# Performance work log

Measured on AMD Instinct MI355X. Metric: run time of the kernel, lower is better.

The kernel has to match this reference:

```python
import jax, jax.numpy as jnp
import numpy as np

B, S, D, H = 4, 2048, 512, 8
NEG_INF = -1e9


def setup_inputs() -> dict:
    key = jax.random.key(0)
    ks = jax.random.split(key, 5)
    x = jax.random.normal(ks[0], (B, S, D), dtype=jnp.float32)
    mask = jnp.ones((B, S), dtype=jnp.int32)
    sc = 0.04  # ~1/sqrt(D) init scale
    Wq = jax.random.normal(ks[1], (H, D, D), dtype=jnp.float32) * sc
    Wk = jax.random.normal(ks[2], (H, D, D), dtype=jnp.float32) * sc
    Wv = jax.random.normal(ks[3], (H, D, D), dtype=jnp.float32) * sc
    Wp = jax.random.normal(ks[4], (D, H * D), dtype=jnp.float32) * sc
    return {"x": x, "mask": mask, "Wq": Wq, "Wk": Wk, "Wv": Wv, "Wp": Wp}


def reference(x, mask, Wq, Wk, Wv, Wp):
    d = x.shape[-1]
    scale = 1.0 / jnp.sqrt(jnp.asarray(d, dtype=jnp.float32))
    # torch Linear: y = x @ W.T ; per-head full-width projections
    q = jnp.einsum("bsd,hed->bhse", x, Wq)  # [B,H,S,D]
    k = jnp.einsum("bsd,hed->bhse", x, Wk)
    v = jnp.einsum("bsd,hed->bhse", x, Wv)
    logits = jnp.einsum("bhse,bhte->bhst", q, k) * scale  # [B,H,S,S]
    # pairwise mask = outer product mask[:,:,None] @ mask[:,None,:]
    pair = (mask[:, :, None] * mask[:, None, :])[:, None, :, :]  # [B,1,S,S]
    logits = jnp.where(pair > 0, logits, NEG_INF)
    attn = jax.nn.softmax(logits, axis=-1)
    out = jnp.einsum("bhst,bhte->bhse", attn, v)  # [B,H,S,D]
    # concat heads along last dim (head order preserved) then proj (no bias)
    bsz, h, s, dd = out.shape
    cat = jnp.transpose(out, (0, 2, 1, 3)).reshape(bsz, s, h * dd)
    return jnp.einsum("bsf,df->bsd", cat, Wp)
```

## Files before the change

kernel.cpp:

```cpp
#include <hip/hip_runtime.h>
#include <hip/hip_bf16.h>


using bf16x8 = __attribute__((ext_vector_type(8))) short;
using f32x4  = __attribute__((ext_vector_type(4))) float;
typedef unsigned short u16;

__device__ __forceinline__ u16 f2bf(float f) {
  union { float f; unsigned u; } c; c.f = f;
  unsigned r = c.u + 0x7fffu + ((c.u >> 16) & 1u);
  return (u16)(r >> 16);
}

__device__ __forceinline__ void gload16(const void* g, void* l) {
  __builtin_amdgcn_global_load_lds((const __attribute__((address_space(1))) unsigned int*)g,
                                   (__attribute__((address_space(3))) unsigned int*)l, 16, 0, 0);
}

__global__ void k_cvt(const float* __restrict__ s, u16* __restrict__ d, int n4) {
  int i = blockIdx.x * 256 + threadIdx.x;
  if (i >= n4) return;
  float4 v = reinterpret_cast<const float4*>(s)[i];
  ushort4 o;
  o.x = f2bf(v.x); o.y = f2bf(v.y); o.z = f2bf(v.z); o.w = f2bf(v.w);
  reinterpret_cast<ushort4*>(d)[i] = o;
}

__global__ __launch_bounds__(256) void k_gemm_qkv(
    const u16* __restrict__ xb, const u16* __restrict__ w,
    u16* __restrict__ Qc, u16* __restrict__ Kc, u16* __restrict__ VTc,
    int h0, int HC)
{
  __shared__ u16 As[128][32];
  __shared__ u16 Bs[128][32];

  const int m0 = blockIdx.x * 128;
  const int n0 = blockIdx.y * 128;
  const int zz = blockIdx.z;
  const int t  = zz / HC, hr = zz % HC;
  const int h  = h0 + hr;

  const int tid  = threadIdx.x;
  const int lane = tid & 63, wv = tid >> 6;
  const int wr = (wv >> 1) * 64, wc = (wv & 1) * 64;
  const int r16 = lane & 15, kg = lane >> 4;

  const u16* wbase = w + (size_t)(t * 8 + h) * 512 * 512;
  const int strow = tid >> 2;
  const int sc4   = (tid & 3) * 8;

  const u16* gaa = xb    + (size_t)(m0 + strow) * 512 + sc4;
  const u16* gbb = wbase + (size_t)(n0 + strow) * 512 + sc4;
  char* AsB = (char*)&As[0][0] + wv * 1024;
  char* BsB = (char*)&Bs[0][0] + wv * 1024;

  f32x4 acc[4][4];
  f32x4 zero = {0.f, 0.f, 0.f, 0.f};
#pragma unroll
  for (int i = 0; i < 4; ++i)
#pragma unroll
    for (int j = 0; j < 4; ++j) acc[i][j] = zero;

  for (int kt = 0; kt < 16; ++kt) {
    __syncthreads();
    const int ko = kt * 32;
    gload16(gaa + ko,            AsB);
    gload16(gaa + 64 * 512 + ko, AsB + 4096);
    gload16(gbb + ko,            BsB);
    gload16(gbb + 64 * 512 + ko, BsB + 4096);
    __syncthreads();
    bf16x8 af[4], bfv[4];
#pragma unroll
    for (int i = 0; i < 4; ++i) af[i]  = *(const bf16x8*)&As[wr + i * 16 + r16][kg * 8];
#pragma unroll
    for (int j = 0; j < 4; ++j) bfv[j] = *(const bf16x8*)&Bs[wc + j * 16 + r16][kg * 8];
#pragma unroll
    for (int i = 0; i < 4; ++i)
#pragma unroll
      for (int j = 0; j < 4; ++j)
        acc[i][j] = __builtin_amdgcn_mfma_f32_16x16x32_bf16(af[i], bfv[j], acc[i][j], 0, 0, 0);
  }

#pragma unroll
  for (int i = 0; i < 4; ++i) {
    const int mbase = m0 + wr + i * 16 + kg * 4;
    const int b   = mbase >> 11;
    const int sl  = mbase & 2047;
    const int bhc = b * HC + hr;
#pragma unroll
    for (int j = 0; j < 4; ++j) {
      const int col = n0 + wc + j * 16 + r16;
      if (t == 2) {
        ushort4 o;
        o.x = f2bf(acc[i][j][0]); o.y = f2bf(acc[i][j][1]);
        o.z = f2bf(acc[i][j][2]); o.w = f2bf(acc[i][j][3]);
        *(ushort4*)&VTc[((size_t)bhc * 512 + col) * 2048 + sl] = o;
      } else if (t == 1) {
#pragma unroll
        for (int q = 0; q < 4; ++q) {
          const int s   = sl + q;
          const int row = s & 63;
          const size_t idx = ((size_t)bhc << 20)
                           + (size_t)((s >> 6) * 4 + (col >> 7)) * 8192
                           + row * 128 + ((col & 127) ^ ((row & 7) << 3));
          Kc[idx] = f2bf(acc[i][j][q]);
        }
      } else {
#pragma unroll
        for (int q = 0; q < 4; ++q)
          Qc[((size_t)bhc * 2048 + sl + q) * 512 + col] = f2bf(acc[i][j][q]);
      }
    }
  }
}

__global__ __launch_bounds__(256) void k_attn(
    const u16* __restrict__ Qc, const u16* __restrict__ Kc, const u16* __restrict__ VTc,
    const int* __restrict__ mask, u16* __restrict__ catc, int HC)
{
  __shared__ u16  Qs[32 * 512];
  __shared__ u16  Ks[2 * 8192];
  __shared__ float S_lds[32][68];
  __shared__ u16  P_lds[32][72];
  __shared__ float m_run[32], l_run[32], alpha_s[32];

  const int lin = blockIdx.x + (blockIdx.y << 6);
  const int per = (gridDim.y << 6) >> 3;
  const int nl  = (lin & 7) * per + (lin >> 3);
  const int qt  = nl & 63, bhc = nl >> 6;

  const int b = bhc / HC, hr = bhc % HC;
  const int q0 = qt * 32;

  const int tid = threadIdx.x, lane = tid & 63, wv = tid >> 6;
  const int r16 = lane & 15, kg = lane >> 4;

  const u16* Qg = Qc + ((size_t)bhc * 2048 + q0) * 512;
  const u16* Kg = Kc + ((size_t)bhc << 20);
  const u16* Vg = VTc + (size_t)bhc * 512 * 2048;
  const int* mrow = mask + b * 2048;

  for (int s = tid; s < 2048; s += 256) {
    const int row = s >> 6, col = (s & 63) * 8;
    *(int4*)&Qs[row * 512 + (col ^ ((row & 7) << 3))] =
        *(const int4*)(Qg + row * 512 + col);
  }
  if (tid < 32) { m_run[tid] = -__builtin_inff(); l_run[tid] = 0.f; }

  auto kissue = [&](int gi, int cur) {
    const u16* g = Kg + (size_t)gi * 8192 + wv * 2048 + lane * 8;
    u16* l = &Ks[cur * 8192 + wv * 2048];
#pragma unroll
    for (int r = 0; r < 4; ++r)
      gload16(g + r * 512, l + r * 512);
  };

  kissue(0, 0);
  kissue(1, 1);

  asm volatile("s_waitcnt lgkmcnt(0)" ::: "memory");
  __builtin_amdgcn_s_barrier();

  const int sm_row = tid >> 3, sm_c0 = (tid & 7) * 8;
  const int rm = mrow[q0 + sm_row];
  const int krow = wv * 16 + r16;
  const int kswz = (krow & 7) << 3;

  f32x4 acc[2][8];
  f32x4 zero = {0.f, 0.f, 0.f, 0.f};
#pragma unroll
  for (int mi = 0; mi < 2; ++mi)
#pragma unroll
    for (int nf = 0; nf < 8; ++nf) acc[mi][nf] = zero;

  const float scale = 0.044194173824159216f;

  for (int it = 0; it < 32; ++it) {
    const int t0 = it * 64;
    f32x4 sacc[2] = {zero, zero};

#pragma unroll
    for (int c = 0; c < 4; ++c) {
      const int gi = it * 4 + c;
      const int cur = gi & 1;
      asm volatile("s_waitcnt vmcnt(4)" ::: "memory");
      __builtin_amdgcn_s_setprio(1);
#pragma unroll
      for (int ks = 0; ks < 4; ++ks) {
        bf16x8 kb = *(const bf16x8*)&Ks[cur * 8192 + krow * 128 + ((ks * 32 + kg * 8) ^ kswz)];
#pragma unroll
        for (int mi = 0; mi < 2; ++mi) {
          const int qrow = mi * 16 + r16;
          bf16x8 qa = *(const bf16x8*)&Qs[qrow * 512 +
              ((c * 128 + ks * 32 + kg * 8) ^ ((qrow & 7) << 3))];
          sacc[mi] = __builtin_amdgcn_mfma_f32_16x16x32_bf16(qa, kb, sacc[mi], 0, 0, 0);
        }
      }
      __builtin_amdgcn_s_setprio(0);
      if (c == 3) {
#pragma unroll
        for (int mi = 0; mi < 2; ++mi)
#pragma unroll
          for (int q = 0; q < 4; ++q)
            S_lds[mi * 16 + kg * 4 + q][wv * 16 + r16] = sacc[mi][q];
      }
      asm volatile("s_waitcnt lgkmcnt(0)" ::: "memory");
      __builtin_amdgcn_sched_barrier(0);
      if (gi + 2 < 128) kissue(gi + 2, cur);
    }
    __builtin_amdgcn_s_barrier();

    bf16x8 vfrag[2][8];
#pragma unroll
    for (int ks = 0; ks < 2; ++ks)
#pragma unroll
      for (int nf = 0; nf < 8; ++nf)
        vfrag[ks][nf] = *(const bf16x8*)(Vg +
            (size_t)(wv * 128 + nf * 16 + r16) * 2048 + t0 + ks * 32 + kg * 8);

    {
      float4 sA = *(float4*)&S_lds[sm_row][sm_c0];
      float4 sB = *(float4*)&S_lds[sm_row][sm_c0 + 4];
      const int4 cA = *(const int4*)(mrow + t0 + sm_c0);
      const int4 cB = *(const int4*)(mrow + t0 + sm_c0 + 4);
      float s0 = (rm && cA.x) ? sA.x * scale : -1e9f;
      float s1 = (rm && cA.y) ? sA.y * scale : -1e9f;
      float s2 = (rm && cA.z) ? sA.z * scale : -1e9f;
      float s3 = (rm && cA.w) ? sA.w * scale : -1e9f;
      float s4 = (rm && cB.x) ? sB.x * scale : -1e9f;
      float s5 = (rm && cB.y) ? sB.y * scale : -1e9f;
      float s6 = (rm && cB.z) ? sB.z * scale : -1e9f;
      float s7 = (rm && cB.w) ? sB.w * scale : -1e9f;
      float mt = fmaxf(fmaxf(fmaxf(s0, s1), fmaxf(s2, s3)),
                       fmaxf(fmaxf(s4, s5), fmaxf(s6, s7)));
      mt = fmaxf(mt, __shfl_xor(mt, 1));
      mt = fmaxf(mt, __shfl_xor(mt, 2));
      mt = fmaxf(mt, __shfl_xor(mt, 4));
      const float mo = m_run[sm_row];
      const float mn = fmaxf(mo, mt);
      const float al = __expf(mo - mn);
      float p0 = __expf(s0 - mn), p1 = __expf(s1 - mn);
      float p2 = __expf(s2 - mn), p3 = __expf(s3 - mn);
      float p4 = __expf(s4 - mn), p5 = __expf(s5 - mn);
      float p6 = __expf(s6 - mn), p7 = __expf(s7 - mn);
      float ps = ((p0 + p1) + (p2 + p3)) + ((p4 + p5) + (p6 + p7));
      ps += __shfl_xor(ps, 1); ps += __shfl_xor(ps, 2); ps += __shfl_xor(ps, 4);
      ushort4 w0, w1;
      w0.x = f2bf(p0); w0.y = f2bf(p1); w0.z = f2bf(p2); w0.w = f2bf(p3);
      w1.x = f2bf(p4); w1.y = f2bf(p5); w1.z = f2bf(p6); w1.w = f2bf(p7);
      *(ushort4*)&P_lds[sm_row][sm_c0]     = w0;
      *(ushort4*)&P_lds[sm_row][sm_c0 + 4] = w1;
      if ((tid & 7) == 0) {
        m_run[sm_row] = mn;
        l_run[sm_row] = l_run[sm_row] * al + ps;
        alpha_s[sm_row] = al;
      }
    }
    asm volatile("s_waitcnt lgkmcnt(0)" ::: "memory");
    __builtin_amdgcn_s_barrier();

    float alq[2][4];
#pragma unroll
    for (int mi = 0; mi < 2; ++mi)
#pragma unroll
      for (int q = 0; q < 4; ++q) alq[mi][q] = alpha_s[mi * 16 + kg * 4 + q];
#pragma unroll
    for (int mi = 0; mi < 2; ++mi)
#pragma unroll
      for (int nf = 0; nf < 8; ++nf) {
        acc[mi][nf][0] *= alq[mi][0]; acc[mi][nf][1] *= alq[mi][1];
        acc[mi][nf][2] *= alq[mi][2]; acc[mi][nf][3] *= alq[mi][3];
      }
    __builtin_amdgcn_s_setprio(1);
#pragma unroll
    for (int ks = 0; ks < 2; ++ks) {
      bf16x8 pa0 = *(const bf16x8*)&P_lds[r16][ks * 32 + kg * 8];
      bf16x8 pa1 = *(const bf16x8*)&P_lds[16 + r16][ks * 32 + kg * 8];
#pragma unroll
      for (int nf = 0; nf < 8; ++nf) {
        acc[0][nf] = __builtin_amdgcn_mfma_f32_16x16x32_bf16(pa0, vfrag[ks][nf], acc[0][nf], 0, 0, 0);
        acc[1][nf] = __builtin_amdgcn_mfma_f32_16x16x32_bf16(pa1, vfrag[ks][nf], acc[1][nf], 0, 0, 0);
      }
    }
    __builtin_amdgcn_s_setprio(0);
  }

  float rinv[2][4];
#pragma unroll
  for (int mi = 0; mi < 2; ++mi)
#pragma unroll
    for (int q = 0; q < 4; ++q) rinv[mi][q] = 1.0f / l_run[mi * 16 + kg * 4 + q];
  const int ldc = HC * 512;
#pragma unroll
  for (int mi = 0; mi < 2; ++mi)
#pragma unroll
    for (int nf = 0; nf < 8; ++nf) {
      const int col = hr * 512 + wv * 128 + nf * 16 + r16;
#pragma unroll
      for (int q = 0; q < 4; ++q) {
        const int row = b * 2048 + q0 + mi * 16 + kg * 4 + q;
        catc[(size_t)row * ldc + col] = f2bf(acc[mi][nf][q] * rinv[mi][q]);
      }
    }
}

__global__ __launch_bounds__(256) void k_gemm_out(
    const u16* __restrict__ A, const u16* __restrict__ Bw, float* __restrict__ out,
    int HC, int h0, int init)
{
  __shared__ u16 As[128][32];
  __shared__ u16 Bs[128][32];

  const int m0 = blockIdx.x * 128;
  const int n0 = blockIdx.y * 128;
  const int tid = threadIdx.x, lane = tid & 63, wv = tid >> 6;
  const int wr = (wv >> 1) * 64, wc = (wv & 1) * 64;
  const int r16 = lane & 15, kg = lane >> 4;
  const int strow = tid >> 2, sc4 = (tid & 3) * 8;
  const size_t lda = (size_t)HC * 512;
  const int nkt = HC * 16;

  const u16* gaa = A  + (size_t)(m0 + strow) * lda + sc4;
  const u16* gbb = Bw + (size_t)(n0 + strow) * 4096 + h0 * 512 + sc4;
  char* AsB = (char*)&As[0][0] + wv * 1024;
  char* BsB = (char*)&Bs[0][0] + wv * 1024;

  f32x4 acc[4][4];
  f32x4 zero = {0.f, 0.f, 0.f, 0.f};
#pragma unroll
  for (int i = 0; i < 4; ++i)
#pragma unroll
    for (int j = 0; j < 4; ++j) acc[i][j] = zero;

  for (int kt = 0; kt < nkt; ++kt) {
    __syncthreads();
    const int ko = kt * 32;
    gload16(gaa + ko,            AsB);
    gload16(gaa + 64 * lda + ko, AsB + 4096);
    gload16(gbb + ko,            BsB);
    gload16(gbb + (size_t)64 * 4096 + ko, BsB + 4096);
    __syncthreads();
    bf16x8 af[4], bfv[4];
#pragma unroll
    for (int i = 0; i < 4; ++i) af[i]  = *(const bf16x8*)&As[wr + i * 16 + r16][kg * 8];
#pragma unroll
    for (int j = 0; j < 4; ++j) bfv[j] = *(const bf16x8*)&Bs[wc + j * 16 + r16][kg * 8];
#pragma unroll
    for (int i = 0; i < 4; ++i)
#pragma unroll
      for (int j = 0; j < 4; ++j)
        acc[i][j] = __builtin_amdgcn_mfma_f32_16x16x32_bf16(af[i], bfv[j], acc[i][j], 0, 0, 0);
  }

#pragma unroll
  for (int i = 0; i < 4; ++i)
#pragma unroll
    for (int j = 0; j < 4; ++j) {
      const int col = n0 + wc + j * 16 + r16;
#pragma unroll
      for (int q = 0; q < 4; ++q) {
        const int row = m0 + wr + i * 16 + kg * 4 + q;
        if (init) out[(size_t)row * 512 + col] = acc[i][j][q];
        else      out[(size_t)row * 512 + col] += acc[i][j][q];
      }
    }
}

extern "C" void kernel_launch(void* const* d_in, const int* in_sizes, int n_in,
                              void* d_out, int out_size, void* d_ws, size_t ws_size,
                              hipStream_t stream)
{
  (void)in_sizes; (void)n_in; (void)out_size;
  const float* x  = (const float*)d_in[0];
  const int* mask = (const int*)d_in[1];
  const float* Wq = (const float*)d_in[2];
  const float* Wk = (const float*)d_in[3];
  const float* Wv = (const float*)d_in[4];
  const float* Wp = (const float*)d_in[5];

  const size_t MiB = 1024 * 1024;
  int HC = 1;
  if (ws_size >= 24 * MiB + 32 * 8 * MiB)      HC = 8;
  else if (ws_size >= 24 * MiB + 32 * 4 * MiB) HC = 4;
  else if (ws_size >= 24 * MiB + 32 * 2 * MiB) HC = 2;

  char* ws = (char*)d_ws;
  size_t off = 0;
  u16* xb   = (u16*)(ws + off); off += 8 * MiB;
  u16* wqkv = (u16*)(ws + off); off += 12 * MiB;
  u16* wpb  = (u16*)(ws + off); off += 4 * MiB;
  const size_t qsz = (size_t)4 * HC * 2048 * 512 * 2;
  u16* Qc  = (u16*)(ws + off); off += qsz;
  u16* Kc  = (u16*)(ws + off); off += qsz;
  u16* VTc = (u16*)(ws + off); off += qsz;
  u16* catc = (u16*)(ws + off);

  k_cvt<<<4096, 256, 0, stream>>>(x,  xb, 1048576);
  k_cvt<<<2048, 256, 0, stream>>>(Wq, wqkv,           524288);
  k_cvt<<<2048, 256, 0, stream>>>(Wk, wqkv + 2097152, 524288);
  k_cvt<<<2048, 256, 0, stream>>>(Wv, wqkv + 4194304, 524288);
  k_cvt<<<2048, 256, 0, stream>>>(Wp, wpb,            524288);

  for (int h0 = 0; h0 < 8; h0 += HC) {
    k_gemm_qkv<<<dim3(64, 4, 3 * HC), 256, 0, stream>>>(xb, wqkv, Qc, Kc, VTc, h0, HC);
    k_attn<<<dim3(64, 4 * HC), 256, 0, stream>>>(Qc, Kc, VTc, mask, catc, HC);
    k_gemm_out<<<dim3(64, 4), 256, 0, stream>>>(catc, wpb, (float*)d_out, HC, h0, h0 == 0);
  }
}
```

Measured before the change: 1.378 ms.

## Split-K output projection with reduction kernel and new attention block mapping

Adds a split-K variant of the output projection GEMM that divides K=4096 into four 1024-wide slices across blockIdx.z. Each slice writes fp32 partials into the reused Qc buffer, and a separate kernel sums the four partials into the output. This raises the grid from 256 to 1024 blocks to fill more CUs, at the cost of extra partial-buffer traffic and one more launch. It also changes the attention block-to-(head, q-tile) remapping so neighbouring blocks share K/V data differently.

```diff
diff --git a/kernel.cpp b/kernel.cpp
--- a/kernel.cpp
+++ b/kernel.cpp
@@ -125,9 +125,15 @@
   __shared__ float m_run[32], l_run[32], alpha_s[32];
 
   const int lin = blockIdx.x + (blockIdx.y << 6);
-  const int per = (gridDim.y << 6) >> 3;
-  const int nl  = (lin & 7) * per + (lin >> 3);
-  const int qt  = nl & 63, bhc = nl >> 6;
+  int qt, bhc;
+  if (HC >= 2) {
+    const int pxb  = HC >> 1;
+    const int slot = lin >> 3;
+    bhc = (lin & 7) * pxb + (slot >> 6);
+    qt  = slot & 63;
+  } else {
+    qt = lin & 63; bhc = lin >> 6;
+  }
 
   const int b = bhc / HC, hr = bhc % HC;
   const int q0 = qt * 32;
@@ -304,6 +310,81 @@
     }
 }
 
+__global__ __launch_bounds__(256) void k_gemm_out_sk(
+    const u16* __restrict__ A, const u16* __restrict__ Bw, float* __restrict__ partial)
+{
+  __shared__ u16 As[128][32];
+  __shared__ u16 Bs[128][32];
+
+  const int m0 = blockIdx.x * 128;
+  const int n0 = blockIdx.y * 128;
+  const int z  = blockIdx.z;
+  const int tid = threadIdx.x, lane = tid & 63, wv = tid >> 6;
+  const int wr = (wv >> 1) * 64, wc = (wv & 1) * 64;
+  const int r16 = lane & 15, kg = lane >> 4;
+  const int strow = tid >> 2, sc4 = (tid & 3) * 8;
+
+  const u16* gaa = A  + (size_t)(m0 + strow) * 4096 + z * 1024 + sc4;
+  const u16* gbb = Bw + (size_t)(n0 + strow) * 4096 + z * 1024 + sc4;
+  char* AsB = (char*)&As[0][0] + wv * 1024;
+  char* BsB = (char*)&Bs[0][0] + wv * 1024;
+
+  f32x4 acc[4][4];
+  f32x4 zero = {0.f, 0.f, 0.f, 0.f};
+#pragma unroll
+  for (int i = 0; i < 4; ++i)
+#pragma unroll
+    for (int j = 0; j < 4; ++j) acc[i][j] = zero;
+
+  for (int kt = 0; kt < 32; ++kt) {
+    __syncthreads();
+    const int ko = kt * 32;
+    gload16(gaa + ko,                     AsB);
+    gload16(gaa + (size_t)64 * 4096 + ko, AsB + 4096);
+    gload16(gbb + ko,                     BsB);
+    gload16(gbb + (size_t)64 * 4096 + ko, BsB + 4096);
+    __syncthreads();
+    bf16x8 af[4], bfv[4];
+#pragma unroll
+    for (int i = 0; i < 4; ++i) af[i]  = *(const bf16x8*)&As[wr + i * 16 + r16][kg * 8];
+#pragma unroll
+    for (int j = 0; j < 4; ++j) bfv[j] = *(const bf16x8*)&Bs[wc + j * 16 + r16][kg * 8];
+#pragma unroll
+    for (int i = 0; i < 4; ++i)
+#pragma unroll
+      for (int j = 0; j < 4; ++j)
+        acc[i][j] = __builtin_amdgcn_mfma_f32_16x16x32_bf16(af[i], bfv[j], acc[i][j], 0, 0, 0);
+  }
+
+  float* dst = partial + (size_t)z * 4194304;
+#pragma unroll
+  for (int i = 0; i < 4; ++i)
+#pragma unroll
+    for (int j = 0; j < 4; ++j) {
+      const int col = n0 + wc + j * 16 + r16;
+#pragma unroll
+      for (int q = 0; q < 4; ++q) {
+        const int row = m0 + wr + i * 16 + kg * 4 + q;
+        dst[(size_t)row * 512 + col] = acc[i][j][q];
+      }
+    }
+}
+
+__global__ void k_red4(const float* __restrict__ p, float* __restrict__ out, int n4) {
+  int i = blockIdx.x * 256 + threadIdx.x;
+  if (i >= n4) return;
+  float4 a = reinterpret_cast<const float4*>(p)[i];
+  float4 b = reinterpret_cast<const float4*>(p + 4194304)[i];
+  float4 c = reinterpret_cast<const float4*>(p + 8388608)[i];
+  float4 d = reinterpret_cast<const float4*>(p + 12582912)[i];
+  float4 o;
+  o.x = (a.x + b.x) + (c.x + d.x);
+  o.y = (a.y + b.y) + (c.y + d.y);
+  o.z = (a.z + b.z) + (c.z + d.z);
+  o.w = (a.w + b.w) + (c.w + d.w);
+  reinterpret_cast<float4*>(out)[i] = o;
+}
+
 __global__ __launch_bounds__(256) void k_gemm_out(
     const u16* __restrict__ A, const u16* __restrict__ Bw, float* __restrict__ out,
     int HC, int h0, int init)
@@ -404,6 +485,11 @@
   for (int h0 = 0; h0 < 8; h0 += HC) {
     k_gemm_qkv<<<dim3(64, 4, 3 * HC), 256, 0, stream>>>(xb, wqkv, Qc, Kc, VTc, h0, HC);
     k_attn<<<dim3(64, 4 * HC), 256, 0, stream>>>(Qc, Kc, VTc, mask, catc, HC);
-    k_gemm_out<<<dim3(64, 4), 256, 0, stream>>>(catc, wpb, (float*)d_out, HC, h0, h0 == 0);
-  }
-}
+    if (HC == 8) {
+      k_gemm_out_sk<<<dim3(64, 4, 4), 256, 0, stream>>>(catc, wpb, (float*)Qc);
+      k_red4<<<4096, 256, 0, stream>>>((const float*)Qc, (float*)d_out, 1048576);
+    } else {
+      k_gemm_out<<<dim3(64, 4), 256, 0, stream>>>(catc, wpb, (float*)d_out, HC, h0, h0 == 0);
+    }
+  }
+}
```

Measured after the change: 1.381 ms. No clear change (+0.2%).
